# Optimization experiments

Hardware: AMD Instinct MI355X
Metric: run time of the kernel (lower is better)

## Reference

```python
import jax, jax.numpy as jnp
import numpy as np

G, NPG, MAXN = 1024, 40, 51   # graphs, nodes/graph, dense pad size
EPG = 80                       # edges per graph
N, E = G * NPG, G * EPG
D_IN, D_OUT, D_EDGE = 64, 32, 16


def _lin(key, fan_in, shape):
    b = 1.0 / np.sqrt(fan_in)
    return jax.random.uniform(key, shape, jnp.float32, -b, b)


def setup_inputs() -> dict:
    key = jax.random.key(0)
    ks = jax.random.split(key, 24)
    node_features = jax.random.randint(ks[0], (N, 9), 0, 128)
    edge_features = jax.random.randint(ks[1], (E, 3), 0, 8)
    offs = jnp.repeat(jnp.arange(G) * NPG, EPG)
    src = jax.random.randint(ks[2], (E,), 0, NPG) + offs
    dst = jax.random.randint(ks[3], (E,), 0, NPG) + offs
    edge_index = jnp.stack([src, dst])
    batch = jnp.repeat(jnp.arange(G), NPG)
    inp = dict(node_features=node_features, edge_features=edge_features,
               edge_index=edge_index, batch=batch)
    # OGB-style encoders: one embedding table per feature column, summed
    inp['atom_emb'] = jax.random.normal(ks[4], (9, 128, D_IN), jnp.float32) * 0.1
    inp['bond_emb'] = jax.random.normal(ks[5], (3, 8, D_EDGE), jnp.float32) * 0.1
    # edge-conditioned weight MLP: 16 -> 1024 -> 256 -> 64*32 (no bias)
    inp['gW1'] = _lin(ks[6], 16, (16, 1024))
    inp['gW2'] = _lin(ks[7], 1024, (1024, 256))
    inp['gW3'] = _lin(ks[8], 256, (256, D_IN * D_OUT))
    # NNConv root weight + bias
    inp['root'] = _lin(ks[9], D_IN, (D_IN, D_OUT))
    inp['conv_bias'] = jnp.zeros((D_OUT,), jnp.float32)
    # readout MLP: 51*32 -> 256 -> 128 -> 32 -> 8 -> 1
    dims = [MAXN * D_OUT, 256, 128, 32, 8, 1]
    for i in range(5):
        inp[f'mW{i+1}'] = _lin(ks[10 + 2 * i], dims[i], (dims[i], dims[i + 1]))
        inp[f'mb{i+1}'] = _lin(ks[11 + 2 * i], dims[i], (dims[i + 1],))
    return inp


def reference(node_features, edge_features, edge_index, batch,
              atom_emb, bond_emb, gW1, gW2, gW3, root, conv_bias,
              mW1, mb1, mW2, mb2, mW3, mb3, mW4, mb4, mW5, mb5):
    # encoders: sum of per-column embeddings
    x = jnp.sum(atom_emb[jnp.arange(9), node_features], axis=1)      # [N,64]
    e = jnp.sum(bond_emb[jnp.arange(3), edge_features], axis=1)      # [E,16]
    # per-edge weight matrix via MLP
    h = jax.nn.relu(e @ gW1)
    h = jax.nn.relu(h @ gW2)
    w = (h @ gW3).reshape(-1, D_IN, D_OUT)                           # [E,64,32]
    # NNConv: gather src, per-edge matmul, scatter-add to dst, + root + bias
    src, dst = edge_index[0], edge_index[1]
    msg = jnp.einsum('ed,edo->eo', x[src], w)                        # [E,32]
    agg = jax.ops.segment_sum(msg, dst, num_segments=N)              # [N,32]
    out = agg + x @ root + conv_bias
    # to_dense_batch(max_num_nodes=51); exactly NPG nodes per graph, zero-pad
    dense = jnp.zeros((G, MAXN, D_OUT), out.dtype).at[:, :NPG].set(
        out.reshape(G, NPG, D_OUT))
    f = dense.reshape(G, MAXN * D_OUT)                               # [G,1632]
    f = jax.nn.relu(f @ mW1 + mb1)
    f = jax.nn.relu(f @ mW2 + mb2)
    f = jax.nn.relu(f @ mW3 + mb3)
    f = jax.nn.relu(f @ mW4 + mb4)
    return f @ mW5 + mb5                                             # [G,1]
```

## Files before the change

### kernel.cpp

```cpp
#include <hip/hip_runtime.h>

#define NNODES 40960
#define NEDGES 81920
#define NG     1024
#define NCOMBO 512

__global__ void k_etab(const float* __restrict__ bemb, float* __restrict__ etab,
                       int* __restrict__ cnt) {
    int gid = blockIdx.x * blockDim.x + threadIdx.x;
    int c = gid >> 4, j = gid & 15;
    int f0 = c >> 6, f1 = (c >> 3) & 7, f2 = c & 7;
    etab[gid] = bemb[(0 * 8 + f0) * 16 + j] + bemb[(1 * 8 + f1) * 16 + j] +
                bemb[(2 * 8 + f2) * 16 + j];
    if ((gid & 15) == 0) cnt[c] = 0;
}

__global__ void k_hist(const int* __restrict__ ef, int* __restrict__ cid,
                       int* __restrict__ cnt) {
    int e = blockIdx.x * blockDim.x + threadIdx.x;
    if (e >= NEDGES) return;
    int c = (ef[e * 3] << 6) | (ef[e * 3 + 1] << 3) | ef[e * 3 + 2];
    cid[e] = c;
    atomicAdd(&cnt[c], 1);
}

__global__ void k_scan(const int* __restrict__ cnt, int* __restrict__ bstart,
                       int* __restrict__ bfill) {
    __shared__ int s[NCOMBO];
    int t = threadIdx.x;
    int my = cnt[t];
    s[t] = my;
    __syncthreads();
    for (int off = 1; off < NCOMBO; off <<= 1) {
        int v = (t >= off) ? s[t - off] : 0;
        __syncthreads();
        s[t] += v;
        __syncthreads();
    }
    int excl = s[t] - my;
    bstart[t] = excl;
    bfill[t] = excl;
    if (t == NCOMBO - 1) bstart[NCOMBO] = NEDGES;
}

__global__ void k_scatter(const int* __restrict__ cid, const int* __restrict__ src,
                          const int* __restrict__ dst, int* __restrict__ bfill,
                          int2* __restrict__ ebuf) {
    int e = blockIdx.x * blockDim.x + threadIdx.x;
    if (e >= NEDGES) return;
    int pos = atomicAdd(&bfill[cid[e]], 1);
    ebuf[pos] = make_int2(src[e], dst[e]);
}

__global__ __launch_bounds__(256) void k_node(
    const int* __restrict__ nf, const float* __restrict__ emb,
    const float* __restrict__ root, const float* __restrict__ bias,
    float* __restrict__ x, float* __restrict__ out) {
    __shared__ float xs[4][64];
    int t = threadIdx.x;
    int nn = t >> 6, d = t & 63;
    int n = blockIdx.x * 4 + nn;
    const int* nfr = nf + n * 9;
    float acc = 0.f;
#pragma unroll
    for (int c = 0; c < 9; ++c) {
        int idx = nfr[c];
        acc += emb[((c << 7) + idx) * 64 + d];
    }
    x[n * 64 + d] = acc;
    xs[nn][d] = acc;
    __syncthreads();
    int o = t & 31, h = (t >> 5) & 1;
    float s = h ? 0.f : bias[o];
    int k0 = h * 32;
#pragma unroll
    for (int kq = 0; kq < 8; ++kq) {
        float4 xv = *reinterpret_cast<const float4*>(&xs[nn][k0 + kq * 4]);
        s += xv.x * root[(k0 + kq * 4 + 0) * 32 + o];
        s += xv.y * root[(k0 + kq * 4 + 1) * 32 + o];
        s += xv.z * root[(k0 + kq * 4 + 2) * 32 + o];
        s += xv.w * root[(k0 + kq * 4 + 3) * 32 + o];
    }
    s += __shfl_xor(s, 32);
    if (!h) out[n * 32 + o] = s;
}

__global__ void k_gemm_naive(const float* __restrict__ A, const float* __restrict__ B,
                             const float* __restrict__ bias, float* __restrict__ C,
                             int M, int N, int K, int relu) {
    int gid = blockIdx.x * blockDim.x + threadIdx.x;
    if (gid >= M * N) return;
    int m = gid / N, n = gid - m * N;
    const float* a = A + m * K;
    float acc = bias ? bias[n] : 0.f;
    for (int k = 0; k < K; ++k) acc += a[k] * B[k * N + n];
    if (relu) acc = fmaxf(acc, 0.f);
    C[gid] = acc;
}

template <int BM, int BN, int BK, int TM, int TN>
__global__ __launch_bounds__(256)
void k_gemm_tiled(const float* __restrict__ A, const float* __restrict__ B,
                  const float* __restrict__ bias, float* __restrict__ C,
                  float* __restrict__ Cp, int M, int N, int K, int KS, int relu) {
    constexpr int TX = BN / TN;
    constexpr int TY = BM / TM;
    static_assert(TX * TY == 256, "block must be 256 threads");
    __shared__ float As[BK][BM + 4];
    __shared__ float Bs[BK][BN + 4];
    const int tx = threadIdx.x % TX, ty = threadIdx.x / TX;
    const int row0 = blockIdx.y * BM, col0 = blockIdx.x * BN;
    const int z = blockIdx.z;
    const int k_begin = z * KS, k_end = k_begin + KS;

    const int am = threadIdx.x >> 2;
    const int ak = (threadIdx.x & 3) << 2;
    const int bk = threadIdx.x >> 4;
    const int bn = (threadIdx.x & 15) << 2;

    float acc[TM][TN] = {};
    for (int k0 = k_begin; k0 < k_end; k0 += BK) {
        float4 av = *reinterpret_cast<const float4*>(&A[(row0 + am) * K + k0 + ak]);
        float4 bv = *reinterpret_cast<const float4*>(&B[(k0 + bk) * N + col0 + bn]);
        As[ak + 0][am] = av.x;
        As[ak + 1][am] = av.y;
        As[ak + 2][am] = av.z;
        As[ak + 3][am] = av.w;
        *reinterpret_cast<float4*>(&Bs[bk][bn]) = bv;
        __syncthreads();
#pragma unroll
        for (int k = 0; k < BK; ++k) {
            float a[TM], b[TN];
            *reinterpret_cast<float4*>(a) =
                *reinterpret_cast<const float4*>(&As[k][ty * TM]);
            *reinterpret_cast<float4*>(b) =
                *reinterpret_cast<const float4*>(&Bs[k][tx * TN]);
#pragma unroll
            for (int i = 0; i < TM; ++i)
#pragma unroll
                for (int j = 0; j < TN; ++j) acc[i][j] += a[i] * b[j];
        }
        __syncthreads();
    }

    const int MN = M * N;
    if (gridDim.z == 1) {
#pragma unroll
        for (int i = 0; i < TM; ++i) {
            int r = row0 + ty * TM + i;
            float4 v;
            v.x = acc[i][0]; v.y = acc[i][1]; v.z = acc[i][2]; v.w = acc[i][3];
            int c = col0 + tx * TN;
            if (bias) { v.x += bias[c]; v.y += bias[c+1]; v.z += bias[c+2]; v.w += bias[c+3]; }
            if (relu) { v.x = fmaxf(v.x,0.f); v.y = fmaxf(v.y,0.f);
                        v.z = fmaxf(v.z,0.f); v.w = fmaxf(v.w,0.f); }
            *reinterpret_cast<float4*>(&C[r * N + c]) = v;
        }
    } else {
        float* dstp = Cp + z * MN;
#pragma unroll
        for (int i = 0; i < TM; ++i) {
            int r = row0 + ty * TM + i;
            float4 v;
            v.x = acc[i][0]; v.y = acc[i][1]; v.z = acc[i][2]; v.w = acc[i][3];
            *reinterpret_cast<float4*>(&dstp[r * N + col0 + tx * TN]) = v;
        }
    }
}

__global__ void k_reduceK(const float* __restrict__ Cp, const float* __restrict__ bias,
                          float* __restrict__ C, int MN, int N, int nz, int relu) {
    int i4 = (blockIdx.x * 256 + threadIdx.x) * 4;
    if (i4 >= MN) return;
    float4 acc = *reinterpret_cast<const float4*>(&Cp[i4]);
    for (int z = 1; z < nz; ++z) {
        float4 t = *reinterpret_cast<const float4*>(&Cp[z * MN + i4]);
        acc.x += t.x; acc.y += t.y; acc.z += t.z; acc.w += t.w;
    }
    if (bias) {
        int c = i4 % N;
        acc.x += bias[c]; acc.y += bias[c + 1]; acc.z += bias[c + 2]; acc.w += bias[c + 3];
    }
    if (relu) {
        acc.x = fmaxf(acc.x, 0.f); acc.y = fmaxf(acc.y, 0.f);
        acc.z = fmaxf(acc.z, 0.f); acc.w = fmaxf(acc.w, 0.f);
    }
    *reinterpret_cast<float4*>(&C[i4]) = acc;
}

__global__ __launch_bounds__(256) void k_msg2(
    const float* __restrict__ x, const float* __restrict__ wtab,
    const int* __restrict__ bstart, const int2* __restrict__ ebuf,
    float* __restrict__ out) {
    __shared__ float xs[64][64];
    __shared__ int2 es[64];
    const int t = threadIdx.x;
    const int c = blockIdx.y;
    const int beg = bstart[c], cnt = bstart[c + 1] - beg;
    if (cnt == 0) return;
    const int o = t & 31;
    float W[64];
    const float* wp = wtab + (c << 11) + o;
#pragma unroll
    for (int k = 0; k < 64; ++k) W[k] = wp[k << 5];

    for (int chunk = blockIdx.x * 64; chunk < cnt; chunk += gridDim.x * 64) {
        int nE = min(64, cnt - chunk);
        if (t < nE) es[t] = ebuf[beg + chunk + t];
        __syncthreads();
        for (int i = t; i < nE * 64; i += 256) {
            int r = i >> 6, d = i & 63;
            xs[r][d] = x[es[r].x * 64 + d];
        }
        __syncthreads();
        for (int e = t >> 5; e < nE; e += 8) {
            float acc = 0.f;
#pragma unroll
            for (int kq = 0; kq < 16; ++kq) {
                float4 xv = *reinterpret_cast<const float4*>(&xs[e][kq * 4]);
                acc += xv.x * W[kq * 4 + 0] + xv.y * W[kq * 4 + 1] +
                       xv.z * W[kq * 4 + 2] + xv.w * W[kq * 4 + 3];
            }
            atomicAdd(&out[es[e].y * 32 + o], acc);
        }
        __syncthreads();
    }
}

__global__ __launch_bounds__(256) void k_tail(
    const float* __restrict__ f2,
    const float* __restrict__ mW3, const float* __restrict__ mb3,
    const float* __restrict__ mW4, const float* __restrict__ mb4,
    const float* __restrict__ mW5, const float* __restrict__ mb5,
    float* __restrict__ outv) {
    __shared__ float s2[4][128];
    __shared__ float s3[4][32];
    __shared__ float s4[4][8];
    const int w = threadIdx.x >> 6, lane = threadIdx.x & 63;
    const int g = blockIdx.x * 4 + w;
    s2[w][lane] = f2[g * 128 + lane];
    s2[w][64 + lane] = f2[g * 128 + 64 + lane];
    __syncthreads();
    if (lane < 32) {
        float acc = mb3[lane];
#pragma unroll 8
        for (int k = 0; k < 128; ++k) acc += s2[w][k] * mW3[k * 32 + lane];
        s3[w][lane] = fmaxf(acc, 0.f);
    }
    __syncthreads();
    if (lane < 8) {
        float acc = mb4[lane];
#pragma unroll
        for (int k = 0; k < 32; ++k) acc += s3[w][k] * mW4[k * 8 + lane];
        s4[w][lane] = fmaxf(acc, 0.f);
    }
    __syncthreads();
    if (lane == 0) {
        float acc = mb5[0];
#pragma unroll
        for (int k = 0; k < 8; ++k) acc += s4[w][k] * mW5[k];
        outv[g] = acc;
    }
}

extern "C" void kernel_launch(void* const* d_in, const int* in_sizes, int n_in,
                              void* d_out, int out_size, void* d_ws, size_t ws_size,
                              hipStream_t stream) {
    const int*   nf      = (const int*)d_in[0];
    const int*   ef      = (const int*)d_in[1];
    const int*   eidx    = (const int*)d_in[2];
    const float* atom_emb= (const float*)d_in[4];
    const float* bond_emb= (const float*)d_in[5];
    const float* gW1     = (const float*)d_in[6];
    const float* gW2     = (const float*)d_in[7];
    const float* gW3     = (const float*)d_in[8];
    const float* root    = (const float*)d_in[9];
    const float* cbias   = (const float*)d_in[10];
    const float* mW1     = (const float*)d_in[11];
    const float* mb1     = (const float*)d_in[12];
    const float* mW2     = (const float*)d_in[13];
    const float* mb2     = (const float*)d_in[14];
    const float* mW3     = (const float*)d_in[15];
    const float* mb3     = (const float*)d_in[16];
    const float* mW4     = (const float*)d_in[17];
    const float* mb4     = (const float*)d_in[18];
    const float* mW5     = (const float*)d_in[19];
    const float* mb5     = (const float*)d_in[20];

    const int* src = eidx;
    const int* dst = eidx + NEDGES;

    float* ws = (float*)d_ws;
    float* x    = ws;
    float* out  = x + 2621440;
    float* etab = out + 1310720;
    float* h1   = etab + 8192;
    float* h2   = h1 + 524288;
    float* wtab = h2 + 131072;
    float* f1   = wtab + 1048576;
    float* f2   = f1 + 262144;
    float* part = f2 + 131072;
    int*   cnt    = (int*)(part + 2097152);
    int*   bstart = cnt + 512;
    int*   bfill  = bstart + 513;
    int*   cid    = bfill + 512;
    int2*  ebuf   = (int2*)f1;

    k_etab<<<NCOMBO * 16 / 256, 256, 0, stream>>>(bond_emb, etab, cnt);
    k_hist<<<NEDGES / 256, 256, 0, stream>>>(ef, cid, cnt);
    k_scan<<<1, NCOMBO, 0, stream>>>(cnt, bstart, bfill);
    k_scatter<<<NEDGES / 256, 256, 0, stream>>>(cid, src, dst, bfill, ebuf);
    k_node<<<NNODES / 4, 256, 0, stream>>>(nf, atom_emb, root, cbias, x, out);
    k_gemm_naive<<<NCOMBO * 1024 / 256, 256, 0, stream>>>(etab, gW1, nullptr, h1,
                                                          NCOMBO, 1024, 16, 1);
    k_gemm_tiled<64, 64, 16, 4, 4><<<dim3(4, 8, 16), 256, 0, stream>>>(
        h1, gW2, nullptr, nullptr, part, NCOMBO, 256, 1024, 64, 0);
    k_reduceK<<<131072 / 1024, 256, 0, stream>>>(part, nullptr, h2, 131072, 256, 16, 1);
    k_gemm_tiled<64, 64, 16, 4, 4><<<dim3(32, 8, 2), 256, 0, stream>>>(
        h2, gW3, nullptr, nullptr, part, NCOMBO, 2048, 256, 128, 0);
    k_reduceK<<<1048576 / 1024, 256, 0, stream>>>(part, nullptr, wtab, 1048576, 2048, 2, 0);
    k_msg2<<<dim3(3, NCOMBO), 256, 0, stream>>>(x, wtab, bstart, ebuf, out);
    k_gemm_tiled<64, 64, 16, 4, 4><<<dim3(4, 16, 8), 256, 0, stream>>>(
        out, mW1, nullptr, nullptr, part, NG, 256, 1280, 160, 0);
    k_reduceK<<<262144 / 1024, 256, 0, stream>>>(part, mb1, f1, 262144, 256, 8, 1);
    k_gemm_tiled<64, 64, 16, 4, 4><<<dim3(2, 16, 4), 256, 0, stream>>>(
        f1, mW2, nullptr, nullptr, part, NG, 128, 256, 64, 0);
    k_reduceK<<<131072 / 1024, 256, 0, stream>>>(part, mb2, f2, 131072, 128, 4, 1);
    k_tail<<<NG / 4, 256, 0, stream>>>(f2, mW3, mb3, mW4, mb4, mW5, mb5, (float*)d_out);
}
```

Before: 258.0 us.

## Fuse split-K reductions into message and readout kernels, vectorize x gather

The split-K reduction for the edge-weight table is folded into the message kernel, which now sums the two partial slices into shared memory before loading its register weights. The reduction of the first readout layer, the second readout GEMM and its reduction are merged with the tail MLP into one per-graph readout kernel. The x-row gather into shared memory now uses float4 loads. This removes four launches and the intermediate buffer round-trips, at the cost of an extra shared-memory pass per block and a simple per-graph dot-product loop for the 256x128 layer instead of a tiled GEMM.

Result: faster. 250.7 us (-2.9%).

```diff
diff --git a/kernel.cpp b/kernel.cpp
--- a/kernel.cpp
+++ b/kernel.cpp
@@ -189,28 +189,38 @@
 }
 
 __global__ __launch_bounds__(256) void k_msg2(
-    const float* __restrict__ x, const float* __restrict__ wtab,
+    const float* __restrict__ wpart, int MN,
+    const float* __restrict__ x,
     const int* __restrict__ bstart, const int2* __restrict__ ebuf,
     float* __restrict__ out) {
+    __shared__ float Ws[2048];
     __shared__ float xs[64][64];
     __shared__ int2 es[64];
     const int t = threadIdx.x;
     const int c = blockIdx.y;
     const int beg = bstart[c], cnt = bstart[c + 1] - beg;
     if (cnt == 0) return;
+    const float* p0 = wpart + (c << 11);
+    const float* p1 = p0 + MN;
+#pragma unroll
+    for (int i = 0; i < 8; ++i) {
+        int idx = i * 256 + t;
+        Ws[idx] = p0[idx] + p1[idx];
+    }
+    __syncthreads();
     const int o = t & 31;
     float W[64];
-    const float* wp = wtab + (c << 11) + o;
-#pragma unroll
-    for (int k = 0; k < 64; ++k) W[k] = wp[k << 5];
+#pragma unroll
+    for (int k = 0; k < 64; ++k) W[k] = Ws[(k << 5) | o];
 
     for (int chunk = blockIdx.x * 64; chunk < cnt; chunk += gridDim.x * 64) {
         int nE = min(64, cnt - chunk);
         if (t < nE) es[t] = ebuf[beg + chunk + t];
         __syncthreads();
-        for (int i = t; i < nE * 64; i += 256) {
-            int r = i >> 6, d = i & 63;
-            xs[r][d] = x[es[r].x * 64 + d];
+        for (int i = t; i < nE * 16; i += 256) {
+            int r = i >> 4, q = i & 15;
+            reinterpret_cast<float4*>(xs[r])[q] =
+                reinterpret_cast<const float4*>(x + es[r].x * 64)[q];
         }
         __syncthreads();
         for (int e = t >> 5; e < nE; e += 8) {
@@ -227,38 +237,52 @@
     }
 }
 
-__global__ __launch_bounds__(256) void k_tail(
-    const float* __restrict__ f2,
+__global__ __launch_bounds__(256) void k_readout(
+    const float* __restrict__ part, const float* __restrict__ mb1,
+    const float* __restrict__ mW2, const float* __restrict__ mb2,
     const float* __restrict__ mW3, const float* __restrict__ mb3,
     const float* __restrict__ mW4, const float* __restrict__ mb4,
     const float* __restrict__ mW5, const float* __restrict__ mb5,
     float* __restrict__ outv) {
-    __shared__ float s2[4][128];
-    __shared__ float s3[4][32];
-    __shared__ float s4[4][8];
-    const int w = threadIdx.x >> 6, lane = threadIdx.x & 63;
-    const int g = blockIdx.x * 4 + w;
-    s2[w][lane] = f2[g * 128 + lane];
-    s2[w][64 + lane] = f2[g * 128 + 64 + lane];
-    __syncthreads();
-    if (lane < 32) {
-        float acc = mb3[lane];
+    __shared__ float f1s[2][256];
+    __shared__ float f2s[2][128];
+    __shared__ float f3s[2][32];
+    __shared__ float f4s[2][8];
+    const int t = threadIdx.x;
+    const int gg = t >> 7, j = t & 127;
+    const int g = blockIdx.x * 2 + gg;
+    for (int k = j; k < 256; k += 128) {
+        float acc = mb1[k];
+#pragma unroll
+        for (int z = 0; z < 8; ++z) acc += part[z * (NG * 256) + g * 256 + k];
+        f1s[gg][k] = fmaxf(acc, 0.f);
+    }
+    __syncthreads();
+    {
+        float acc = mb2[j];
 #pragma unroll 8
-        for (int k = 0; k < 128; ++k) acc += s2[w][k] * mW3[k * 32 + lane];
-        s3[w][lane] = fmaxf(acc, 0.f);
-    }
-    __syncthreads();
-    if (lane < 8) {
-        float acc = mb4[lane];
-#pragma unroll
-        for (int k = 0; k < 32; ++k) acc += s3[w][k] * mW4[k * 8 + lane];
-        s4[w][lane] = fmaxf(acc, 0.f);
-    }
-    __syncthreads();
-    if (lane == 0) {
+        for (int k = 0; k < 256; ++k) acc += f1s[gg][k] * mW2[k * 128 + j];
+        f2s[gg][j] = fmaxf(acc, 0.f);
+    }
+    __syncthreads();
+    if (j < 32) {
+        float acc = mb3[j];
+#pragma unroll 8
+        for (int k = 0; k < 128; ++k) acc += f2s[gg][k] * mW3[k * 32 + j];
+        f3s[gg][j] = fmaxf(acc, 0.f);
+    }
+    __syncthreads();
+    if (j < 8) {
+        float acc = mb4[j];
+#pragma unroll
+        for (int k = 0; k < 32; ++k) acc += f3s[gg][k] * mW4[k * 8 + j];
+        f4s[gg][j] = fmaxf(acc, 0.f);
+    }
+    __syncthreads();
+    if (j == 0) {
         float acc = mb5[0];
 #pragma unroll
-        for (int k = 0; k < 8; ++k) acc += s4[w][k] * mW5[k];
+        for (int k = 0; k < 8; ++k) acc += f4s[gg][k] * mW5[k];
         outv[g] = acc;
     }
 }
@@ -296,15 +320,13 @@
     float* etab = out + 1310720;
     float* h1   = etab + 8192;
     float* h2   = h1 + 524288;
-    float* wtab = h2 + 131072;
-    float* f1   = wtab + 1048576;
-    float* f2   = f1 + 262144;
-    float* part = f2 + 131072;
+    float* dead = h2 + 131072;
+    float* part = dead + 1048576 + 262144 + 131072;
     int*   cnt    = (int*)(part + 2097152);
     int*   bstart = cnt + 512;
     int*   bfill  = bstart + 513;
     int*   cid    = bfill + 512;
-    int2*  ebuf   = (int2*)f1;
+    int2*  ebuf   = (int2*)dead;
 
     k_etab<<<NCOMBO * 16 / 256, 256, 0, stream>>>(bond_emb, etab, cnt);
     k_hist<<<NEDGES / 256, 256, 0, stream>>>(ef, cid, cnt);
@@ -318,13 +340,9 @@
     k_reduceK<<<131072 / 1024, 256, 0, stream>>>(part, nullptr, h2, 131072, 256, 16, 1);
     k_gemm_tiled<64, 64, 16, 4, 4><<<dim3(32, 8, 2), 256, 0, stream>>>(
         h2, gW3, nullptr, nullptr, part, NCOMBO, 2048, 256, 128, 0);
-    k_reduceK<<<1048576 / 1024, 256, 0, stream>>>(part, nullptr, wtab, 1048576, 2048, 2, 0);
-    k_msg2<<<dim3(3, NCOMBO), 256, 0, stream>>>(x, wtab, bstart, ebuf, out);
+    k_msg2<<<dim3(3, NCOMBO), 256, 0, stream>>>(part, NCOMBO * 2048, x, bstart, ebuf, out);
     k_gemm_tiled<64, 64, 16, 4, 4><<<dim3(4, 16, 8), 256, 0, stream>>>(
         out, mW1, nullptr, nullptr, part, NG, 256, 1280, 160, 0);
-    k_reduceK<<<262144 / 1024, 256, 0, stream>>>(part, mb1, f1, 262144, 256, 8, 1);
-    k_gemm_tiled<64, 64, 16, 4, 4><<<dim3(2, 16, 4), 256, 0, stream>>>(
-        f1, mW2, nullptr, nullptr, part, NG, 128, 256, 64, 0);
-    k_reduceK<<<131072 / 1024, 256, 0, stream>>>(part, mb2, f2, 131072, 128, 4, 1);
-    k_tail<<<NG / 4, 256, 0, stream>>>(f2, mW3, mb3, mW4, mb4, mW5, mb5, (float*)d_out);
-}
+    k_readout<<<NG / 2, 256, 0, stream>>>(part, mb1, mW2, mb2, mW3, mb3,
+                                          mW4, mb4, mW5, mb5, (float*)d_out);
+}
```
